# Kernel tuning notes

Hardware: AMD Instinct MI355X
Metric: run time of the kernel (lower is better)

The kernel has to match this reference:

```python
import jax, jax.numpy as jnp
import numpy as np

N = 8192       # batch_size
D = 128        # embedding dim
C = 1000       # num classes
EPS = 1e-8     # torch CosineSimilarity eps


def setup_inputs() -> dict:
    key = jax.random.key(0)
    k1, k2, k3, k4 = jax.random.split(key, 4)
    inst_embed = jax.random.normal(k1, (N, D), dtype=jnp.float32)
    proxy = jax.random.normal(k2, (N, D), dtype=jnp.float32)
    # binary mask marking same-class (non-negative) pairs, stored as float
    negative_mask = (jax.random.uniform(k3, (N, C)) < 0.5).astype(jnp.float32)
    labels = jax.random.randint(k4, (N,), 0, C)
    temperature = jnp.float32(0.07)
    margin = jnp.float32(0.0)
    return {
        'inst_embed': inst_embed,
        'proxy': proxy,
        'negative_mask': negative_mask,
        'labels': labels,
        'temperature': temperature,
        'margin': margin,
    }


def _remove_diag(M):
    # M: [h, h] -> [h, h-1], dropping the diagonal, row-major order (as torch bool-mask view)
    h = M.shape[0]
    j = jnp.arange(h - 1)[None, :]
    i = jnp.arange(h)[:, None]
    cols = j + (j >= i)  # skip column i in row i
    return jnp.take_along_axis(M, cols, axis=1)


def _l2_normalize(x):
    return x / jnp.maximum(jnp.linalg.norm(x, axis=-1, keepdims=True), EPS)


def reference(inst_embed, proxy, negative_mask, labels, temperature, margin):
    negative_mask = negative_mask.T                       # [C, N]
    xn = _l2_normalize(inst_embed)                        # [N, D]
    sim = xn @ xn.T                                       # [N, N] cosine similarity matrix
    instance_zone = jnp.exp((_remove_diag(sim) - margin) / temperature)  # [N, N-1]
    pn = _l2_normalize(proxy)
    inst2proxy_positive = jnp.exp((jnp.sum(xn * pn, axis=-1) - margin) / temperature)  # [N]
    # pos_collected_numerator == True branch
    mask_4_remove_negatives = _remove_diag(negative_mask[labels])        # [N, N-1]
    inst2inst_positives = instance_zone * mask_4_remove_negatives
    numerator = inst2proxy_positive + inst2inst_positives.sum(axis=1)
    denominator = inst2proxy_positive + instance_zone.sum(axis=1)
    criterion = -jnp.log(temperature * (numerator / denominator)).mean()
    return criterion
```

## Files before the change

kernel.cpp:

```cpp
#include <hip/hip_runtime.h>
#include <hip/hip_bf16.h>

typedef unsigned short u16;
typedef unsigned int   u32;
typedef unsigned long long u64;
typedef __attribute__((ext_vector_type(8))) short short8;
typedef __attribute__((ext_vector_type(4))) float float4v;

#define N 8192
#define D 128
#define C 1000
#define TILE 128
#define NW64 (N / 64)
#define JQ 8
#define JW (JQ * 2)
#define LOG2E 1.44269504088896340736f

__global__ void prep_kernel(const float* __restrict__ nm, u64* __restrict__ packed,
                            const float* __restrict__ x, const float* __restrict__ pr,
                            u16* __restrict__ xnb, float* __restrict__ p_out,
                            float* __restrict__ den, float* __restrict__ num,
                            const float* __restrict__ tp, const float* __restrict__ mp) {
    __shared__ u32 Ls[64 * 65];
    const int bid  = blockIdx.x;
    const int lane = threadIdx.x & 63;
    const int wv   = threadIdx.x >> 6;

    if (bid < 2048) {
        const int jt = bid & 127;
        const int lt = bid >> 7;
        const int j0 = jt * 64;
        const int l  = lt * 64 + lane;
        const bool lv = l < C;

        #pragma unroll
        for (int rr = 0; rr < 16; rr++) {
            const int r = wv * 16 + rr;
            float v = lv ? nm[(size_t)(j0 + r) * C + l] : 0.0f;
            Ls[r * 65 + lane] = (v > 0.5f) ? 1u : 0u;
        }
        __syncthreads();
        #pragma unroll
        for (int cc = 0; cc < 16; cc++) {
            const int c = wv * 16 + cc;
            u64 m = __ballot(Ls[lane * 65 + c] != 0u);
            if (lane == 0 && (lt * 64 + c) < C)
                packed[(size_t)(lt * 64 + c) * NW64 + jt] = m;
        }
    } else {
        const int row = (bid - 2048) * 4 + wv;
        const float2* xr  = (const float2*)(x  + (size_t)row * D);
        const float2* prr = (const float2*)(pr + (size_t)row * D);
        float2 xv = xr[lane];
        float2 pv = prr[lane];

        float sx  = xv.x * xv.x + xv.y * xv.y;
        float sp  = pv.x * pv.x + pv.y * pv.y;
        float sxp = xv.x * pv.x + xv.y * pv.y;
        #pragma unroll
        for (int off = 32; off; off >>= 1) {
            sx  += __shfl_xor(sx,  off);
            sp  += __shfl_xor(sp,  off);
            sxp += __shfl_xor(sxp, off);
        }
        float nx = fmaxf(sqrtf(sx), 1e-8f);
        float np = fmaxf(sqrtf(sp), 1e-8f);
        float inv = 1.0f / nx;

        __hip_bfloat16 b0 = __float2bfloat16(xv.x * inv);
        __hip_bfloat16 b1 = __float2bfloat16(xv.y * inv);
        ((__hip_bfloat162*)xnb)[(size_t)row * 64 + lane] = __halves2bfloat162(b0, b1);

        if (lane == 0) {
            float T = tp[0], M = mp[0];
            p_out[row] = __expf((sxp / (nx * np) - M) / T);
            den[row] = 0.0f;
            num[row] = 0.0f;
        }
    }
}

template <bool RELOAD>
__device__ __forceinline__ void mfma_half(float4v (&acc)[4][2], const short8 (&a_f)[4][4],
                                          short8 (&bc)[4][2], const u16* __restrict__ Bnext) {
    #pragma unroll
    for (int a = 0; a < 4; a++)
        #pragma unroll
        for (int b = 0; b < 2; b++)
            acc[a][b] = (float4v){0.f, 0.f, 0.f, 0.f};
    #pragma unroll
    for (int kk = 0; kk < 4; kk++) {
        #pragma unroll
        for (int tm = 0; tm < 4; tm++)
            #pragma unroll
            for (int tn = 0; tn < 2; tn++)
                acc[tm][tn] = __builtin_amdgcn_mfma_f32_16x16x32_bf16(
                    a_f[kk][tm], bc[kk][tn], acc[tm][tn], 0, 0, 0);
        if (RELOAD) {
            #pragma unroll
            for (int tn = 0; tn < 2; tn++)
                bc[kk][tn] = *(const short8*)(Bnext + tn * (16 * D) + kk * 32);
        }
    }
}

template <bool DIAG, int H>
__device__ __forceinline__ void epi_half(const float4v (&acc)[4][2], const u64* __restrict__ Ms,
                                         float (&dacc)[4][4], float (&nacc)[4][4],
                                         int wr, int wc, int kq, int m0,
                                         int ibase, int jbase, int q,
                                         float kA2, float kB2) {
    #pragma unroll
    for (int tm = 0; tm < 4; tm++) {
        #pragma unroll
        for (int r = 0; r < 4; r++) {
            const int lrow = wr * 64 + tm * 16 + kq * 4 + r;
            const u64 ws = Ms[lrow * JW + q * 2 + wc] >> m0;
            const int gi = ibase + lrow;
            #pragma unroll
            for (int tn = 0; tn < 2; tn++) {
                float e = __builtin_amdgcn_exp2f(fmaf(acc[tm][tn][r], kA2, kB2));
                if (DIAG) {
                    const int gj = jbase + wc * 64 + (H * 2 + tn) * 16 + m0;
                    if (gi == gj) e = 0.0f;
                }
                dacc[tm][r] += e;
                const u32 bit = (u32)(ws >> ((H * 2 + tn) * 16)) & 1u;
                nacc[tm][r] = fmaf((float)bit, e, nacc[tm][r]);
            }
        }
    }
}

__global__ __launch_bounds__(256, 2)
void cc_main(const u16* __restrict__ xnb, const int* __restrict__ labels,
             const u64* __restrict__ packed,
             float* __restrict__ den, float* __restrict__ num,
             const float* __restrict__ tp, const float* __restrict__ mp) {
    __shared__ u64 Ms[TILE * JW];

    const int tid  = threadIdx.x;
    const int lane = tid & 63;
    const int wv   = tid >> 6;
    const int wr   = wv >> 1;
    const int wc   = wv & 1;
    const int m0   = lane & 15;
    const int kq   = lane >> 4;
    const int ibase  = blockIdx.x * TILE;
    const int jsplit = blockIdx.y;
    const int jt0    = jsplit * JQ;

    const float T = tp[0];
    const float M = mp[0];
    const float kA2 = LOG2E / T;
    const float kB2 = -M * LOG2E / T;

    #pragma unroll
    for (int t = 0; t < 8; t++) {
        const int idx = t * 256 + tid;
        const int row = idx >> 4, h = idx & 15;
        const int lab = labels[ibase + row];
        Ms[idx] = packed[(size_t)lab * NW64 + jt0 * 2 + h];
    }

    const u16* Alane = xnb + (size_t)(ibase + wr * 64 + m0) * D + kq * 8;
    short8 a_f[4][4];
    #pragma unroll
    for (int kk = 0; kk < 4; kk++)
        #pragma unroll
        for (int tm = 0; tm < 4; tm++)
            a_f[kk][tm] = *(const short8*)(Alane + tm * (16 * D) + kk * 32);

    __syncthreads();

    float dacc[4][4] = {};
    float nacc[4][4] = {};

    const u16* Blane = xnb + (size_t)(wc * 64 + m0) * D + kq * 8;

    float4v acc[4][2];
    short8 bc[4][2];

    {
        const u16* B0 = Blane + (size_t)(jt0 * TILE) * D;
        #pragma unroll
        for (int kk = 0; kk < 4; kk++)
            #pragma unroll
            for (int tn = 0; tn < 2; tn++)
                bc[kk][tn] = *(const short8*)(B0 + tn * (16 * D) + kk * 32);
    }

    for (int q = 0; q < JQ; q++) {
        const int jt = jt0 + q;
        const int jbase = jt * TILE;
        const u16* Bq = Blane + (size_t)jbase * D;
        const bool diag = (jt == blockIdx.x);

        mfma_half<true>(acc, a_f, bc, Bq + 32 * D);
        if (diag) epi_half<true , 0>(acc, Ms, dacc, nacc, wr, wc, kq, m0, ibase, jbase, q, kA2, kB2);
        else      epi_half<false, 0>(acc, Ms, dacc, nacc, wr, wc, kq, m0, ibase, jbase, q, kA2, kB2);

        if (q < JQ - 1) mfma_half<true >(acc, a_f, bc, Bq + TILE * D);
        else            mfma_half<false>(acc, a_f, bc, Bq + TILE * D);
        if (diag) epi_half<true , 1>(acc, Ms, dacc, nacc, wr, wc, kq, m0, ibase, jbase, q, kA2, kB2);
        else      epi_half<false, 1>(acc, Ms, dacc, nacc, wr, wc, kq, m0, ibase, jbase, q, kA2, kB2);
    }

    #pragma unroll
    for (int tm = 0; tm < 4; tm++) {
        #pragma unroll
        for (int r = 0; r < 4; r++) {
            float d = dacc[tm][r], n = nacc[tm][r];
            #pragma unroll
            for (int off = 1; off < 16; off <<= 1) {
                d += __shfl_xor(d, off);
                n += __shfl_xor(n, off);
            }
            if (m0 == 0) {
                const int gi = ibase + wr * 64 + tm * 16 + kq * 4 + r;
                atomicAdd(&den[gi], d);
                atomicAdd(&num[gi], n);
            }
        }
    }
}

__global__ void loss_kernel(const float* __restrict__ p, const float* __restrict__ den,
                            const float* __restrict__ num, float* __restrict__ out,
                            const float* __restrict__ tp) {
    __shared__ float red[16];
    const float T = tp[0];
    float s = 0.0f;
    #pragma unroll
    for (int t = 0; t < N / 1024; t++) {
        const int i = t * 1024 + threadIdx.x;
        float pi = p[i];
        s += -__logf(T * (pi + num[i]) / (pi + den[i]));
    }
    #pragma unroll
    for (int off = 32; off; off >>= 1) s += __shfl_xor(s, off);
    const int lane = threadIdx.x & 63, wv = threadIdx.x >> 6;
    if (lane == 0) red[wv] = s;
    __syncthreads();
    if (wv == 0) {
        float t = (lane < 16) ? red[lane] : 0.0f;
        #pragma unroll
        for (int off = 8; off; off >>= 1) t += __shfl_xor(t, off);
        if (lane == 0) out[0] = t / (float)N;
    }
}

extern "C" void kernel_launch(void* const* d_in, const int* in_sizes, int n_in,
                              void* d_out, int out_size, void* d_ws, size_t ws_size,
                              hipStream_t stream) {
    (void)in_sizes; (void)n_in; (void)out_size; (void)ws_size;
    const float* inst   = (const float*)d_in[0];
    const float* proxy  = (const float*)d_in[1];
    const float* nm     = (const float*)d_in[2];
    const int*   labels = (const int*)d_in[3];
    const float* temp   = (const float*)d_in[4];
    const float* marg   = (const float*)d_in[5];
    float* out = (float*)d_out;

    char* ws = (char*)d_ws;
    u16*   xnb    = (u16*)ws;
    float* p_arr  = (float*)(ws + 2097152);
    u64*   packed = (u64*)(ws + 2129920);
    float* den    = (float*)(ws + 3153920);
    float* num    = (float*)(ws + 3186688);

    prep_kernel<<<4096, 256, 0, stream>>>(nm, packed, inst, proxy, xnb, p_arr,
                                          den, num, temp, marg);
    cc_main<<<dim3(N / TILE, 8), 256, 0, stream>>>(xnb, labels, packed, den, num, temp, marg);
    loss_kernel<<<1, 1024, 0, stream>>>(p_arr, den, num, out, temp);
}
```

Before: 140.9 us.

## Split 128x128 tile across waves by rows, each wave sweeping all columns

Changes the warp-level decomposition from a 2x2 grid of 64x64 wave tiles to four 32-row strips, each wave covering all 128 columns in four 32-column chunks. This halves per-wave A-fragment and accumulator registers, which may allow more latency hiding. The trade-off is that every wave now loads the full B tile from global memory, doubling B traffic per block, and issues more but smaller MFMA/epilogue rounds.

New measurement: 158.9 us. 12.8% more time.

```diff
diff --git a/kernel.cpp b/kernel.cpp
--- a/kernel.cpp
+++ b/kernel.cpp
@@ -81,17 +81,17 @@
 }
 
 template <bool RELOAD>
-__device__ __forceinline__ void mfma_half(float4v (&acc)[4][2], const short8 (&a_f)[4][4],
-                                          short8 (&bc)[4][2], const u16* __restrict__ Bnext) {
-    #pragma unroll
-    for (int a = 0; a < 4; a++)
+__device__ __forceinline__ void mfma_chunk(float4v (&acc)[2][2], const short8 (&a_f)[4][2],
+                                           short8 (&bc)[4][2], const u16* __restrict__ Bnext) {
+    #pragma unroll
+    for (int a = 0; a < 2; a++)
         #pragma unroll
         for (int b = 0; b < 2; b++)
             acc[a][b] = (float4v){0.f, 0.f, 0.f, 0.f};
     #pragma unroll
     for (int kk = 0; kk < 4; kk++) {
         #pragma unroll
-        for (int tm = 0; tm < 4; tm++)
+        for (int tm = 0; tm < 2; tm++)
             #pragma unroll
             for (int tn = 0; tn < 2; tn++)
                 acc[tm][tn] = __builtin_amdgcn_mfma_f32_16x16x32_bf16(
@@ -104,28 +104,28 @@
     }
 }
 
-template <bool DIAG, int H>
-__device__ __forceinline__ void epi_half(const float4v (&acc)[4][2], const u64* __restrict__ Ms,
-                                         float (&dacc)[4][4], float (&nacc)[4][4],
-                                         int wr, int wc, int kq, int m0,
-                                         int ibase, int jbase, int q,
-                                         float kA2, float kB2) {
-    #pragma unroll
-    for (int tm = 0; tm < 4; tm++) {
+template <bool DIAG, int CI>
+__device__ __forceinline__ void epi_chunk(const float4v (&acc)[2][2], const u64* __restrict__ Ms,
+                                          float (&dacc)[2][4], float (&nacc)[2][4],
+                                          int wv, int kq, int m0,
+                                          int ibase, int jbase, int q,
+                                          float kA2, float kB2) {
+    #pragma unroll
+    for (int tm = 0; tm < 2; tm++) {
         #pragma unroll
         for (int r = 0; r < 4; r++) {
-            const int lrow = wr * 64 + tm * 16 + kq * 4 + r;
-            const u64 ws = Ms[lrow * JW + q * 2 + wc] >> m0;
+            const int lrow = wv * 32 + tm * 16 + kq * 4 + r;
+            const u64 ws = Ms[lrow * JW + q * 2 + (CI >> 1)] >> m0;
             const int gi = ibase + lrow;
             #pragma unroll
             for (int tn = 0; tn < 2; tn++) {
                 float e = __builtin_amdgcn_exp2f(fmaf(acc[tm][tn][r], kA2, kB2));
                 if (DIAG) {
-                    const int gj = jbase + wc * 64 + (H * 2 + tn) * 16 + m0;
+                    const int gj = jbase + CI * 32 + tn * 16 + m0;
                     if (gi == gj) e = 0.0f;
                 }
                 dacc[tm][r] += e;
-                const u32 bit = (u32)(ws >> ((H * 2 + tn) * 16)) & 1u;
+                const u32 bit = (u32)(ws >> (((CI & 1) * 2 + tn) * 16)) & 1u;
                 nacc[tm][r] = fmaf((float)bit, e, nacc[tm][r]);
             }
         }
@@ -142,8 +142,6 @@
     const int tid  = threadIdx.x;
     const int lane = tid & 63;
     const int wv   = tid >> 6;
-    const int wr   = wv >> 1;
-    const int wc   = wv & 1;
     const int m0   = lane & 15;
     const int kq   = lane >> 4;
     const int ibase  = blockIdx.x * TILE;
@@ -163,22 +161,22 @@
         Ms[idx] = packed[(size_t)lab * NW64 + jt0 * 2 + h];
     }
 
-    const u16* Alane = xnb + (size_t)(ibase + wr * 64 + m0) * D + kq * 8;
-    short8 a_f[4][4];
+    const u16* Alane = xnb + (size_t)(ibase + wv * 32 + m0) * D + kq * 8;
+    short8 a_f[4][2];
     #pragma unroll
     for (int kk = 0; kk < 4; kk++)
         #pragma unroll
-        for (int tm = 0; tm < 4; tm++)
+        for (int tm = 0; tm < 2; tm++)
             a_f[kk][tm] = *(const short8*)(Alane + tm * (16 * D) + kk * 32);
 
     __syncthreads();
 
-    float dacc[4][4] = {};
-    float nacc[4][4] = {};
-
-    const u16* Blane = xnb + (size_t)(wc * 64 + m0) * D + kq * 8;
-
-    float4v acc[4][2];
+    float dacc[2][4] = {};
+    float nacc[2][4] = {};
+
+    const u16* Blane = xnb + (size_t)m0 * D + kq * 8;
+
+    float4v acc[2][2];
     short8 bc[4][2];
 
     {
@@ -196,18 +194,26 @@
         const u16* Bq = Blane + (size_t)jbase * D;
         const bool diag = (jt == blockIdx.x);
 
-        mfma_half<true>(acc, a_f, bc, Bq + 32 * D);
-        if (diag) epi_half<true , 0>(acc, Ms, dacc, nacc, wr, wc, kq, m0, ibase, jbase, q, kA2, kB2);
-        else      epi_half<false, 0>(acc, Ms, dacc, nacc, wr, wc, kq, m0, ibase, jbase, q, kA2, kB2);
-
-        if (q < JQ - 1) mfma_half<true >(acc, a_f, bc, Bq + TILE * D);
-        else            mfma_half<false>(acc, a_f, bc, Bq + TILE * D);
-        if (diag) epi_half<true , 1>(acc, Ms, dacc, nacc, wr, wc, kq, m0, ibase, jbase, q, kA2, kB2);
-        else      epi_half<false, 1>(acc, Ms, dacc, nacc, wr, wc, kq, m0, ibase, jbase, q, kA2, kB2);
-    }
-
-    #pragma unroll
-    for (int tm = 0; tm < 4; tm++) {
+        mfma_chunk<true>(acc, a_f, bc, Bq + 32 * D);
+        if (diag) epi_chunk<true , 0>(acc, Ms, dacc, nacc, wv, kq, m0, ibase, jbase, q, kA2, kB2);
+        else      epi_chunk<false, 0>(acc, Ms, dacc, nacc, wv, kq, m0, ibase, jbase, q, kA2, kB2);
+
+        mfma_chunk<true>(acc, a_f, bc, Bq + 64 * D);
+        if (diag) epi_chunk<true , 1>(acc, Ms, dacc, nacc, wv, kq, m0, ibase, jbase, q, kA2, kB2);
+        else      epi_chunk<false, 1>(acc, Ms, dacc, nacc, wv, kq, m0, ibase, jbase, q, kA2, kB2);
+
+        mfma_chunk<true>(acc, a_f, bc, Bq + 96 * D);
+        if (diag) epi_chunk<true , 2>(acc, Ms, dacc, nacc, wv, kq, m0, ibase, jbase, q, kA2, kB2);
+        else      epi_chunk<false, 2>(acc, Ms, dacc, nacc, wv, kq, m0, ibase, jbase, q, kA2, kB2);
+
+        if (q < JQ - 1) mfma_chunk<true >(acc, a_f, bc, Bq + 128 * D);
+        else            mfma_chunk<false>(acc, a_f, bc, Bq + 128 * D);
+        if (diag) epi_chunk<true , 3>(acc, Ms, dacc, nacc, wv, kq, m0, ibase, jbase, q, kA2, kB2);
+        else      epi_chunk<false, 3>(acc, Ms, dacc, nacc, wv, kq, m0, ibase, jbase, q, kA2, kB2);
+    }
+
+    #pragma unroll
+    for (int tm = 0; tm < 2; tm++) {
         #pragma unroll
         for (int r = 0; r < 4; r++) {
             float d = dacc[tm][r], n = nacc[tm][r];
@@ -217,7 +223,7 @@
                 n += __shfl_xor(n, off);
             }
             if (m0 == 0) {
-                const int gi = ibase + wr * 64 + tm * 16 + kq * 4 + r;
+                const int gi = ibase + wv * 32 + tm * 16 + kq * 4 + r;
                 atomicAdd(&den[gi], d);
                 atomicAdd(&num[gi], n);
             }
```
